# Optimization experiments

Measured on AMD Instinct MI355X. Metric: run time of the kernel, lower is better.

The kernel has to match this reference:

```python
import jax, jax.numpy as jnp
import numpy as np

B, C, H, W = 4, 512, 64, 64
KEY_DIM, VALUE_DIM = 512, 512


def setup_inputs() -> dict:
    key = jax.random.key(0)
    k1, k2, k3, k4 = jax.random.split(key, 4)
    s = 1.0 / np.sqrt(C).astype(np.float32)
    x = jax.random.normal(k1, (B, C, H, W), jnp.float32)
    # torch nn.Linear weights have shape (out_features, in_features)
    Wk = jax.random.normal(k2, (KEY_DIM, C), jnp.float32) * s
    Wq = jax.random.normal(k3, (KEY_DIM, C), jnp.float32) * s
    Wv = jax.random.normal(k4, (VALUE_DIM, C), jnp.float32) * s
    return {"x": x, "Wk": Wk, "Wq": Wq, "Wv": Wv}


def reference(x, Wk, Wq, Wv):
    b, c, h, w = x.shape
    kd = Wk.shape[0]
    n = h * w
    # (b,c,h,w) -> (b, n, c) tokens, matching transpose+flatten in the original
    xt = x.transpose(0, 2, 3, 1).reshape(b, n, c)
    q = xt @ Wq.T  # (b, n, kd)
    k = xt @ Wk.T  # (b, n, kd)
    v = xt @ Wv.T  # (b, n, vd)
    scaling = np.sqrt(float(kd)).astype(np.float32)
    scores = jax.nn.softmax(jnp.einsum('bnd,bmd->bnm', q, k) / scaling, axis=-1)
    # original: output[j] = sum_i values[i] * scores[j, i]  ==  scores @ V
    out = jnp.einsum('bnm,bmv->bnv', scores, v)  # (b, n, vd)
    # original scores_out: sum over dim=0 (query index) of the (n, n) score matrix
    scores_out = scores.sum(axis=1).reshape(b, 1, h, w)
    out = out.reshape(b, h, w, -1).transpose(0, 3, 1, 2)  # (b, vd, h, w)
    return out, scores_out
```

## Files before the change

### kernel.cpp

```cpp
#include <hip/hip_runtime.h>


typedef short bf16x8 __attribute__((ext_vector_type(8)));
typedef float f32x4 __attribute__((ext_vector_type(4)));

#define NTOK 4096
#define DDIM 512
#define NB   4

__device__ __forceinline__ unsigned short f32_bf16(float f) {
  union { float f; unsigned u; } v; v.f = f;
  unsigned r = v.u + 0x7FFFu + ((v.u >> 16) & 1u);
  return (unsigned short)(r >> 16);
}

__device__ __forceinline__ float bf16_f32(short s) {
  union { unsigned u; float f; } v;
  v.u = ((unsigned)(unsigned short)s) << 16;
  return v.f;
}

__global__ __launch_bounds__(256, 4) void qkv_proj(
    const float* __restrict__ x,
    const float* __restrict__ Wq,
    const float* __restrict__ Wk,
    const float* __restrict__ Wv,
    unsigned short* __restrict__ Qt,
    unsigned short* __restrict__ Kf,
    unsigned short* __restrict__ Vt)
{
  const int nt0 = blockIdx.x * 64;
  const int d0  = blockIdx.y * 64;
  const int b   = blockIdx.z;
  const int tid = threadIdx.x;
  const int wave = tid >> 6;
  const int lane = tid & 63;
  const int l15  = lane & 15;
  const int quad = lane >> 4;

  __shared__ __align__(16) unsigned short Xt[64 * 40];
  __shared__ __align__(16) unsigned short Wl[3][64 * 40];

  f32x4 aq[4], ak[4], av[4];
#pragma unroll
  for (int i = 0; i < 4; ++i) {
    aq[i] = (f32x4){0.f,0.f,0.f,0.f};
    ak[i] = (f32x4){0.f,0.f,0.f,0.f};
    av[i] = (f32x4){0.f,0.f,0.f,0.f};
  }

  const float* xb = x + (size_t)b * DDIM * NTOK + nt0;
  const int xn  = tid & 63;
  const int xc8 = tid >> 6;
  const int wc8 = tid & 3;
  const int wdd = tid >> 2;

  for (int cc = 0; cc < DDIM; cc += 32) {
    __syncthreads();
    {
      bf16x8 t;
#pragma unroll
      for (int j = 0; j < 8; ++j)
        t[j] = (short)f32_bf16(xb[(size_t)(cc + xc8 * 8 + j) * NTOK + xn]);
      *(bf16x8*)(&Xt[xn * 40 + xc8 * 8]) = t;
    }
    {
      const float* wsrc[3] = {Wq, Wk, Wv};
#pragma unroll
      for (int m = 0; m < 3; ++m) {
        const float* src = wsrc[m] + (size_t)(d0 + wdd) * DDIM + cc + wc8 * 8;
        bf16x8 t;
#pragma unroll
        for (int j = 0; j < 8; ++j) t[j] = (short)f32_bf16(src[j]);
        *(bf16x8*)(&Wl[m][wdd * 40 + wc8 * 8]) = t;
      }
    }
    __syncthreads();

    bf16x8 xa  = *(const bf16x8*)(&Xt[(wave * 16 + l15) * 40 + quad * 8]);
    bf16x8 wva = *(const bf16x8*)(&Wl[2][(wave * 16 + l15) * 40 + quad * 8]);
#pragma unroll
    for (int nt = 0; nt < 4; ++nt) {
      bf16x8 wqf = *(const bf16x8*)(&Wl[0][(nt * 16 + l15) * 40 + quad * 8]);
      bf16x8 wkf = *(const bf16x8*)(&Wl[1][(nt * 16 + l15) * 40 + quad * 8]);
      bf16x8 xbf = *(const bf16x8*)(&Xt[(nt * 16 + l15) * 40 + quad * 8]);
      aq[nt] = __builtin_amdgcn_mfma_f32_16x16x32_bf16(xa,  wqf, aq[nt], 0, 0, 0);
      ak[nt] = __builtin_amdgcn_mfma_f32_16x16x32_bf16(xa,  wkf, ak[nt], 0, 0, 0);
      av[nt] = __builtin_amdgcn_mfma_f32_16x16x32_bf16(wva, xbf, av[nt], 0, 0, 0);
    }
  }

#pragma unroll
  for (int nt = 0; nt < 4; ++nt) {
#pragma unroll
    for (int r = 0; r < 4; ++r) {
      const int tokq = nt0 + wave * 16 + quad * 4 + r;
      const int dq   = d0 + nt * 16 + l15;
      Qt[((size_t)b * NTOK + tokq) * DDIM + dq] = f32_bf16(aq[nt][r]);
      {
        const int kblk  = (nt0 >> 4) + wave;
        const int dc    = (d0 >> 5) + (nt >> 1);
        const int laneK = ((nt & 1) * 2 + (l15 >> 3)) * 16 + quad * 4 + r;
        Kf[((size_t)(b * 256 + kblk) * 16 + dc) * 512 + laneK * 8 + (l15 & 7)] =
            f32_bf16(ak[nt][r]);
      }
      const int dblk  = (d0 >> 4) + wave;
      const int ic    = (nt0 >> 5) + (nt >> 1);
      const int laneV = ((nt & 1) * 2 + (l15 >> 3)) * 16 + quad * 4 + r;
      Vt[(size_t)b * DDIM * NTOK +
         ((size_t)(dblk * 128 + ic) * 64 + laneV) * 8 + (l15 & 7)] =
          f32_bf16(av[nt][r]);
    }
  }
}

#define SCALE 0.044194173824159216f

__global__ __launch_bounds__(256, 2) void attn_lsum_p(
    const unsigned short* __restrict__ Qt,
    const unsigned short* __restrict__ Kf,
    unsigned short* __restrict__ Pt,
    float* __restrict__ lsum_g)
{
  const int qb = blockIdx.x;
  const int kp = blockIdx.y;
  const int b  = blockIdx.z;
  const int tid  = threadIdx.x;
  const int wave = tid >> 6;
  const int lane = tid & 63;
  const int l15  = lane & 15;
  const int quad = lane >> 4;
  const int q0   = qb * 128 + wave * 32;

  __shared__ __align__(16) unsigned short Klds[64 * 512];

  bf16x8 qf[2][16];
#pragma unroll
  for (int qt = 0; qt < 2; ++qt) {
    const unsigned short* qp =
        Qt + ((size_t)b * NTOK + q0 + qt * 16 + l15) * DDIM + quad * 8;
#pragma unroll
    for (int dc = 0; dc < 16; ++dc) qf[qt][dc] = *(const bf16x8*)(qp + dc * 32);
  }

  unsigned short* Pq = Pt + (size_t)b * NTOK * NTOK +
                       (size_t)(qb * 2 + (wave >> 1)) * 262144;
  const int ntb = (wave & 1) * 2;

  float ls[2][4] = {{0.f,0.f,0.f,0.f},{0.f,0.f,0.f,0.f}};

  for (int kc = 0; kc < 16; ++kc) {
    const int kblk0 = kp * 64 + kc * 4;
    __syncthreads();
    {
      const unsigned short* src = Kf + ((size_t)(b * 256 + kblk0) * 16) * 512;
#pragma unroll
      for (int it = 0; it < 16; ++it) {
        const int idx = (tid + it * 256) * 8;
        *(bf16x8*)(&Klds[idx]) = *(const bf16x8*)(src + idx);
      }
    }
    __syncthreads();

#pragma unroll
    for (int kt = 0; kt < 4; ++kt) {
      const int kabs = kblk0 + kt;
      f32x4 s0 = (f32x4){0.f,0.f,0.f,0.f};
      f32x4 s1 = (f32x4){0.f,0.f,0.f,0.f};
#pragma unroll
      for (int dc = 0; dc < 16; ++dc) {
        const bf16x8 kbf = *(const bf16x8*)(&Klds[(kt * 16 + dc) * 512 + lane * 8]);
        s0 = __builtin_amdgcn_mfma_f32_16x16x32_bf16(qf[0][dc], kbf, s0, 0, 0, 0);
        s1 = __builtin_amdgcn_mfma_f32_16x16x32_bf16(qf[1][dc], kbf, s1, 0, 0, 0);
      }
      const int ic    = kabs >> 1;
      const int lt_hi = ((kabs & 1) * 2 + (l15 >> 3)) * 16;
      const int jj    = l15 & 7;
#pragma unroll
      for (int r = 0; r < 4; ++r) {
        const float e0 = __expf(s0[r] * SCALE);
        const float e1 = __expf(s1[r] * SCALE);
        ls[0][r] += e0;
        ls[1][r] += e1;
        Pq[((size_t)(ic * 4 + ntb) * 64 + lt_hi + quad * 4 + r) * 8 + jj] =
            f32_bf16(e0);
        Pq[((size_t)(ic * 4 + ntb + 1) * 64 + lt_hi + quad * 4 + r) * 8 + jj] =
            f32_bf16(e1);
      }
    }
  }

#pragma unroll
  for (int qt = 0; qt < 2; ++qt)
#pragma unroll
    for (int r = 0; r < 4; ++r) {
      float v = ls[qt][r];
      v += __shfl_xor(v, 1);
      v += __shfl_xor(v, 2);
      v += __shfl_xor(v, 4);
      v += __shfl_xor(v, 8);
      if (l15 == 0)
        unsafeAtomicAdd(&lsum_g[(size_t)b * NTOK + q0 + qt * 16 + quad * 4 + r], v);
    }
}

__global__ __launch_bounds__(256, 2) void attn_pv(
    const unsigned short* __restrict__ Pt,
    const unsigned short* __restrict__ Vt,
    const float* __restrict__ lsum_g,
    float* __restrict__ out)
{
  const int q0b   = blockIdx.x;
  const int dpart = blockIdx.y;
  const int b     = blockIdx.z;
  const int tid  = threadIdx.x;
  const int wave = tid >> 6;
  const int lane = tid & 63;
  const int l15  = lane & 15;
  const int quad = lane >> 4;

  const int dblk0 = dpart * 16 + wave * 4;
  const unsigned short* Pq =
      Pt + (size_t)b * NTOK * NTOK + (size_t)q0b * 262144 + lane * 8;
  const unsigned short* Vb =
      Vt + (size_t)b * DDIM * NTOK + lane * 8;

  float rlv[4];
#pragma unroll
  for (int nt = 0; nt < 4; ++nt)
    rlv[nt] = 1.0f / lsum_g[(size_t)b * NTOK + q0b * 64 + nt * 16 + l15];

  f32x4 o[4][4];
#pragma unroll
  for (int i = 0; i < 4; ++i)
#pragma unroll
    for (int j = 0; j < 4; ++j) o[i][j] = (f32x4){0.f,0.f,0.f,0.f};

  bf16x8 pc[4], vc[4], pn[4], vn[4];
#pragma unroll
  for (int nt = 0; nt < 4; ++nt)
    pc[nt] = *(const bf16x8*)(Pq + (size_t)nt * 512);
#pragma unroll
  for (int mt = 0; mt < 4; ++mt)
    vc[mt] = *(const bf16x8*)(Vb + (size_t)(dblk0 + mt) * 65536);

#pragma unroll 2
  for (int ic = 0; ic < 127; ++ic) {
#pragma unroll
    for (int nt = 0; nt < 4; ++nt)
      pn[nt] = *(const bf16x8*)(Pq + (size_t)(ic + 1) * 2048 + (size_t)nt * 512);
#pragma unroll
    for (int mt = 0; mt < 4; ++mt)
      vn[mt] = *(const bf16x8*)(Vb + (size_t)(dblk0 + mt) * 65536 + (size_t)(ic + 1) * 512);
#pragma unroll
    for (int mt = 0; mt < 4; ++mt)
#pragma unroll
      for (int nt = 0; nt < 4; ++nt)
        o[mt][nt] = __builtin_amdgcn_mfma_f32_16x16x32_bf16(vc[mt], pc[nt], o[mt][nt], 0, 0, 0);
#pragma unroll
    for (int nt = 0; nt < 4; ++nt) pc[nt] = pn[nt];
#pragma unroll
    for (int mt = 0; mt < 4; ++mt) vc[mt] = vn[mt];
  }
#pragma unroll
  for (int mt = 0; mt < 4; ++mt)
#pragma unroll
    for (int nt = 0; nt < 4; ++nt)
      o[mt][nt] = __builtin_amdgcn_mfma_f32_16x16x32_bf16(vc[mt], pc[nt], o[mt][nt], 0, 0, 0);

  float* ob = out + ((size_t)b * DDIM + dpart * 256 + wave * 64) * NTOK + q0b * 64;
#pragma unroll
  for (int mt = 0; mt < 4; ++mt)
#pragma unroll
    for (int nt = 0; nt < 4; ++nt)
#pragma unroll
      for (int r = 0; r < 4; ++r)
        ob[(size_t)(mt * 16 + quad * 4 + r) * NTOK + nt * 16 + l15] =
            o[mt][nt][r] * rlv[nt];
}

__global__ __launch_bounds__(256, 4) void colsum_k(
    const unsigned short* __restrict__ Pt,
    const float* __restrict__ lsum_g,
    float* __restrict__ scores_out)
{
  const int ic = blockIdx.x;
  const int b  = blockIdx.y;
  const int tid = threadIdx.x;
  const int wave = tid >> 6;
  const int lane = tid & 63;
  const int l15  = lane & 15;
  const int quad = lane >> 4;

  __shared__ float red[4][32];

  const unsigned short* Pb = Pt + (size_t)b * NTOK * NTOK + (size_t)ic * 2048 + lane * 8;
  const float* lb = lsum_g + (size_t)b * NTOK;

  float acc[8];
#pragma unroll
  for (int j = 0; j < 8; ++j) acc[j] = 0.f;

  for (int q0b = wave; q0b < 64; q0b += 4) {
    const unsigned short* src = Pb + (size_t)q0b * 262144;
#pragma unroll
    for (int nt = 0; nt < 4; ++nt) {
      const bf16x8 p = *(const bf16x8*)(src + (size_t)nt * 512);
      const float rl = 1.0f / lb[q0b * 64 + nt * 16 + l15];
#pragma unroll
      for (int j = 0; j < 8; ++j) acc[j] = fmaf(bf16_f32(p[j]), rl, acc[j]);
    }
  }
#pragma unroll
  for (int j = 0; j < 8; ++j) {
    float v = acc[j];
    v += __shfl_xor(v, 1);
    v += __shfl_xor(v, 2);
    v += __shfl_xor(v, 4);
    v += __shfl_xor(v, 8);
    acc[j] = v;
  }
  if (l15 == 0) {
#pragma unroll
    for (int j = 0; j < 8; ++j) red[wave][quad * 8 + j] = acc[j];
  }
  __syncthreads();
  if (tid < 32)
    scores_out[(size_t)b * NTOK + ic * 32 + tid] =
        red[0][tid] + red[1][tid] + red[2][tid] + red[3][tid];
}

extern "C" void kernel_launch(void* const* d_in, const int* in_sizes, int n_in,
                              void* d_out, int out_size, void* d_ws, size_t ws_size,
                              hipStream_t stream) {
  const float* x  = (const float*)d_in[0];
  const float* Wk = (const float*)d_in[1];
  const float* Wq = (const float*)d_in[2];
  const float* Wv = (const float*)d_in[3];

  float* out = (float*)d_out;
  float* scores_out = out + (size_t)NB * DDIM * NTOK;

  const size_t mat_elems = (size_t)NB * NTOK * DDIM;
  unsigned short* Qt = (unsigned short*)d_ws;
  unsigned short* Kf = Qt + mat_elems;
  unsigned short* Vt = Kf + mat_elems;
  float* lbuf = (float*)(Vt + mat_elems);
  unsigned short* Pt = (unsigned short*)(lbuf + (size_t)NB * NTOK);

  hipMemsetAsync(lbuf, 0, (size_t)NB * NTOK * sizeof(float), stream);

  dim3 g1(NTOK / 64, DDIM / 64, NB);
  qkv_proj<<<g1, 256, 0, stream>>>(x, Wq, Wk, Wv, Qt, Kf, Vt);

  dim3 g2(NTOK / 128, 4, NB);
  attn_lsum_p<<<g2, 256, 0, stream>>>(Qt, Kf, Pt, lbuf);

  dim3 g3(NTOK / 64, 2, NB);
  attn_pv<<<g3, 256, 0, stream>>>(Pt, Vt, lbuf, out);

  dim3 g4(128, NB);
  colsum_k<<<g4, 256, 0, stream>>>(Pt, lbuf, scores_out);
}
```

Baseline: 358.6 us.

## Fuse column-sum into PV kernel and shrink per-wave output tile

Removes the separate colsum kernel by computing the softmax column sums inside attn_pv, with each P chunk summed by exactly one wave and accumulated via atomics into a zero-initialized scores buffer. The PV tile per wave is halved (2 d-blocks instead of 4), the grid doubles along the d dimension, and launch bounds allow higher occupancy, with explicit double-buffered loads. This saves one kernel launch and the dedicated pass over P for column sums. In exchange each P tile is now read by twice as many blocks, and atomics plus an extra memset are added.

```diff
diff --git a/kernel.cpp b/kernel.cpp
--- a/kernel.cpp
+++ b/kernel.cpp
@@ -204,11 +204,12 @@
     }
 }
 
-__global__ __launch_bounds__(256, 2) void attn_pv(
+__global__ __launch_bounds__(256, 4) void attn_pv(
     const unsigned short* __restrict__ Pt,
     const unsigned short* __restrict__ Vt,
     const float* __restrict__ lsum_g,
-    float* __restrict__ out)
+    float* __restrict__ out,
+    float* __restrict__ scores_out)
 {
   const int q0b   = blockIdx.x;
   const int dpart = blockIdx.y;
@@ -219,115 +220,96 @@
   const int l15  = lane & 15;
   const int quad = lane >> 4;
 
-  const int dblk0 = dpart * 16 + wave * 4;
+  const int dblk0 = dpart * 8 + wave * 2;
   const unsigned short* Pq =
       Pt + (size_t)b * NTOK * NTOK + (size_t)q0b * 262144 + lane * 8;
-  const unsigned short* Vb =
-      Vt + (size_t)b * DDIM * NTOK + lane * 8;
+  const unsigned short* Vp0 =
+      Vt + (size_t)b * DDIM * NTOK + (size_t)(dblk0 + 0) * 65536 + lane * 8;
+  const unsigned short* Vp1 =
+      Vt + (size_t)b * DDIM * NTOK + (size_t)(dblk0 + 1) * 65536 + lane * 8;
+  float* scb = scores_out + (size_t)b * NTOK;
 
   float rlv[4];
 #pragma unroll
   for (int nt = 0; nt < 4; ++nt)
     rlv[nt] = 1.0f / lsum_g[(size_t)b * NTOK + q0b * 64 + nt * 16 + l15];
 
-  f32x4 o[4][4];
-#pragma unroll
-  for (int i = 0; i < 4; ++i)
+  f32x4 o[2][4];
+#pragma unroll
+  for (int i = 0; i < 2; ++i)
 #pragma unroll
     for (int j = 0; j < 4; ++j) o[i][j] = (f32x4){0.f,0.f,0.f,0.f};
 
-  bf16x8 pc[4], vc[4], pn[4], vn[4];
-#pragma unroll
-  for (int nt = 0; nt < 4; ++nt)
-    pc[nt] = *(const bf16x8*)(Pq + (size_t)nt * 512);
-#pragma unroll
-  for (int mt = 0; mt < 4; ++mt)
-    vc[mt] = *(const bf16x8*)(Vb + (size_t)(dblk0 + mt) * 65536);
-
-#pragma unroll 2
-  for (int ic = 0; ic < 127; ++ic) {
-#pragma unroll
-    for (int nt = 0; nt < 4; ++nt)
-      pn[nt] = *(const bf16x8*)(Pq + (size_t)(ic + 1) * 2048 + (size_t)nt * 512);
-#pragma unroll
-    for (int mt = 0; mt < 4; ++mt)
-      vn[mt] = *(const bf16x8*)(Vb + (size_t)(dblk0 + mt) * 65536 + (size_t)(ic + 1) * 512);
-#pragma unroll
-    for (int mt = 0; mt < 4; ++mt)
-#pragma unroll
-      for (int nt = 0; nt < 4; ++nt)
-        o[mt][nt] = __builtin_amdgcn_mfma_f32_16x16x32_bf16(vc[mt], pc[nt], o[mt][nt], 0, 0, 0);
-#pragma unroll
-    for (int nt = 0; nt < 4; ++nt) pc[nt] = pn[nt];
-#pragma unroll
-    for (int mt = 0; mt < 4; ++mt) vc[mt] = vn[mt];
-  }
-#pragma unroll
-  for (int mt = 0; mt < 4; ++mt)
-#pragma unroll
-    for (int nt = 0; nt < 4; ++nt)
-      o[mt][nt] = __builtin_amdgcn_mfma_f32_16x16x32_bf16(vc[mt], pc[nt], o[mt][nt], 0, 0, 0);
-
-  float* ob = out + ((size_t)b * DDIM + dpart * 256 + wave * 64) * NTOK + q0b * 64;
-#pragma unroll
-  for (int mt = 0; mt < 4; ++mt)
+  bf16x8 pA[4], pB[4], vA[2], vB[2];
+
+#define LOADP(D_, IC_)                                                         \
+  do {                                                                         \
+    _Pragma("unroll") for (int nt = 0; nt < 4; ++nt)                           \
+      D_[nt] = *(const bf16x8*)(Pq + (size_t)(IC_)*2048 + nt * 512);           \
+  } while (0)
+
+#define LOADV(D_, IC_)                                                         \
+  do {                                                                         \
+    D_[0] = *(const bf16x8*)(Vp0 + (size_t)(IC_)*512);                         \
+    D_[1] = *(const bf16x8*)(Vp1 + (size_t)(IC_)*512);                         \
+  } while (0)
+
+#define PV_COMPUTE(P_, V_, IC_)                                                \
+  do {                                                                         \
+    _Pragma("unroll") for (int mt = 0; mt < 2; ++mt)                           \
+      _Pragma("unroll") for (int nt = 0; nt < 4; ++nt)                         \
+        o[mt][nt] = __builtin_amdgcn_mfma_f32_16x16x32_bf16(                   \
+            V_[mt], P_[nt], o[mt][nt], 0, 0, 0);                               \
+    if ((((IC_) >> 5) == dpart) && ((((IC_) >> 3) & 3) == wave)) {             \
+      float cj[8];                                                             \
+      _Pragma("unroll") for (int j = 0; j < 8; ++j) cj[j] = 0.f;               \
+      _Pragma("unroll") for (int nt = 0; nt < 4; ++nt)                         \
+        _Pragma("unroll") for (int j = 0; j < 8; ++j)                          \
+          cj[j] = fmaf(bf16_f32(P_[nt][j]), rlv[nt], cj[j]);                   \
+      _Pragma("unroll") for (int j = 0; j < 8; ++j) {                          \
+        float v_ = cj[j];                                                      \
+        v_ += __shfl_xor(v_, 1);                                               \
+        v_ += __shfl_xor(v_, 2);                                               \
+        v_ += __shfl_xor(v_, 4);                                               \
+        v_ += __shfl_xor(v_, 8);                                               \
+        cj[j] = v_;                                                            \
+      }                                                                        \
+      if (l15 == 0) {                                                          \
+        _Pragma("unroll") for (int j = 0; j < 8; ++j)                          \
+          unsafeAtomicAdd(&scb[(IC_)*32 + quad * 8 + j], cj[j]);               \
+      }                                                                        \
+    }                                                                          \
+  } while (0)
+
+  LOADP(pA, 0); LOADV(vA, 0);
+  LOADP(pB, 1); LOADV(vB, 1);
+
+  for (int ic = 0; ic < 124; ic += 2) {
+    PV_COMPUTE(pA, vA, ic);
+    LOADP(pA, ic + 2); LOADV(vA, ic + 2);
+    PV_COMPUTE(pB, vB, ic + 1);
+    LOADP(pB, ic + 3); LOADV(vB, ic + 3);
+  }
+  PV_COMPUTE(pA, vA, 124);
+  LOADP(pA, 126); LOADV(vA, 126);
+  PV_COMPUTE(pB, vB, 125);
+  LOADP(pB, 127); LOADV(vB, 127);
+  PV_COMPUTE(pA, vA, 126);
+  PV_COMPUTE(pB, vB, 127);
+
+#undef LOADP
+#undef LOADV
+#undef PV_COMPUTE
+
+  float* ob = out + ((size_t)b * DDIM + dpart * 128 + wave * 32) * NTOK + q0b * 64;
+#pragma unroll
+  for (int mt = 0; mt < 2; ++mt)
 #pragma unroll
     for (int nt = 0; nt < 4; ++nt)
 #pragma unroll
       for (int r = 0; r < 4; ++r)
         ob[(size_t)(mt * 16 + quad * 4 + r) * NTOK + nt * 16 + l15] =
             o[mt][nt][r] * rlv[nt];
-}
-
-__global__ __launch_bounds__(256, 4) void colsum_k(
-    const unsigned short* __restrict__ Pt,
-    const float* __restrict__ lsum_g,
-    float* __restrict__ scores_out)
-{
-  const int ic = blockIdx.x;
-  const int b  = blockIdx.y;
-  const int tid = threadIdx.x;
-  const int wave = tid >> 6;
-  const int lane = tid & 63;
-  const int l15  = lane & 15;
-  const int quad = lane >> 4;
-
-  __shared__ float red[4][32];
-
-  const unsigned short* Pb = Pt + (size_t)b * NTOK * NTOK + (size_t)ic * 2048 + lane * 8;
-  const float* lb = lsum_g + (size_t)b * NTOK;
-
-  float acc[8];
-#pragma unroll
-  for (int j = 0; j < 8; ++j) acc[j] = 0.f;
-
-  for (int q0b = wave; q0b < 64; q0b += 4) {
-    const unsigned short* src = Pb + (size_t)q0b * 262144;
-#pragma unroll
-    for (int nt = 0; nt < 4; ++nt) {
-      const bf16x8 p = *(const bf16x8*)(src + (size_t)nt * 512);
-      const float rl = 1.0f / lb[q0b * 64 + nt * 16 + l15];
-#pragma unroll
-      for (int j = 0; j < 8; ++j) acc[j] = fmaf(bf16_f32(p[j]), rl, acc[j]);
-    }
-  }
-#pragma unroll
-  for (int j = 0; j < 8; ++j) {
-    float v = acc[j];
-    v += __shfl_xor(v, 1);
-    v += __shfl_xor(v, 2);
-    v += __shfl_xor(v, 4);
-    v += __shfl_xor(v, 8);
-    acc[j] = v;
-  }
-  if (l15 == 0) {
-#pragma unroll
-    for (int j = 0; j < 8; ++j) red[wave][quad * 8 + j] = acc[j];
-  }
-  __syncthreads();
-  if (tid < 32)
-    scores_out[(size_t)b * NTOK + ic * 32 + tid] =
-        red[0][tid] + red[1][tid] + red[2][tid] + red[3][tid];
 }
 
 extern "C" void kernel_launch(void* const* d_in, const int* in_sizes, int n_in,
@@ -349,6 +331,7 @@
   unsigned short* Pt = (unsigned short*)(lbuf + (size_t)NB * NTOK);
 
   hipMemsetAsync(lbuf, 0, (size_t)NB * NTOK * sizeof(float), stream);
+  hipMemsetAsync(scores_out, 0, (size_t)NB * NTOK * sizeof(float), stream);
 
   dim3 g1(NTOK / 64, DDIM / 64, NB);
   qkv_proj<<<g1, 256, 0, stream>>>(x, Wq, Wk, Wv, Qt, Kf, Vt);
@@ -356,9 +339,6 @@
   dim3 g2(NTOK / 128, 4, NB);
   attn_lsum_p<<<g2, 256, 0, stream>>>(Qt, Kf, Pt, lbuf);
 
-  dim3 g3(NTOK / 64, 2, NB);
-  attn_pv<<<g3, 256, 0, stream>>>(Pt, Vt, lbuf, out);
-
-  dim3 g4(128, NB);
-  colsum_k<<<g4, 256, 0, stream>>>(Pt, lbuf, scores_out);
-}
+  dim3 g3(NTOK / 64, 4, NB);
+  attn_pv<<<g3, 256, 0, stream>>>(Pt, Vt, lbuf, out, scores_out);
+}
```

Result: slower. 404.8 us (+12.9%).

## Double-buffer K and P tiles in LDS via async global_load_lds

Applied to the files above, without the earlier changes.

The QK^T kernel now stages K chunks into a double-buffered LDS array with direct global-to-LDS loads, so the next chunk is prefetched while MFMAs run on the current one. This replaces two barriers per chunk with one. The PV kernel stops loading P straight into registers from global memory and instead stages P tiles through double-buffered LDS with async loads. V fragments are kept in two rotating register sets. This adds 64KB of LDS per block in the PV kernel, which may lower occupancy.

```diff
diff --git a/kernel.cpp b/kernel.cpp
--- a/kernel.cpp
+++ b/kernel.cpp
@@ -18,6 +18,13 @@
   union { unsigned u; float f; } v;
   v.u = ((unsigned)(unsigned short)s) << 16;
   return v.f;
+}
+
+__device__ __forceinline__ void gload_lds16(const unsigned short* g,
+                                            unsigned short* l) {
+  __builtin_amdgcn_global_load_lds(
+      (__attribute__((address_space(1))) void*)(g),
+      (__attribute__((address_space(3))) void*)(l), 16, 0, 0);
 }
 
 __global__ __launch_bounds__(256, 4) void qkv_proj(
@@ -132,7 +139,7 @@
   const int quad = lane >> 4;
   const int q0   = qb * 128 + wave * 32;
 
-  __shared__ __align__(16) unsigned short Klds[64 * 512];
+  __shared__ __align__(16) unsigned short Klds[2][16384];
 
   bf16x8 qf[2][16];
 #pragma unroll
@@ -149,27 +156,33 @@
 
   float ls[2][4] = {{0.f,0.f,0.f,0.f},{0.f,0.f,0.f,0.f}};
 
-  for (int kc = 0; kc < 16; ++kc) {
-    const int kblk0 = kp * 64 + kc * 4;
-    __syncthreads();
-    {
-      const unsigned short* src = Kf + ((size_t)(b * 256 + kblk0) * 16) * 512;
-#pragma unroll
-      for (int it = 0; it < 16; ++it) {
-        const int idx = (tid + it * 256) * 8;
-        *(bf16x8*)(&Klds[idx]) = *(const bf16x8*)(src + idx);
-      }
-    }
-    __syncthreads();
-
-#pragma unroll
-    for (int kt = 0; kt < 4; ++kt) {
-      const int kabs = kblk0 + kt;
+  const unsigned short* Ksrc0 = Kf + ((size_t)(b * 256 + kp * 64) * 16) * 512;
+
+#define KSTAGE(KC_, B_)                                                        \
+  do {                                                                         \
+    const unsigned short* ks_ = Ksrc0 + (size_t)(KC_)*16384;                   \
+    _Pragma("unroll") for (int c_ = 0; c_ < 8; ++c_) {                         \
+      const int ch_ = c_ * 4 + wave;                                           \
+      gload_lds16(ks_ + ch_ * 512 + lane * 8, &Klds[B_][ch_ * 512]);           \
+    }                                                                          \
+  } while (0)
+
+  KSTAGE(0, 0);
+  __syncthreads();
+
+  for (int kc2 = 0; kc2 < 32; ++kc2) {
+    const int cb = kc2 & 1;
+    if (kc2 < 31) KSTAGE(kc2 + 1, cb ^ 1);
+
+#pragma unroll
+    for (int kt = 0; kt < 2; ++kt) {
+      const int kabs = kp * 64 + kc2 * 2 + kt;
       f32x4 s0 = (f32x4){0.f,0.f,0.f,0.f};
       f32x4 s1 = (f32x4){0.f,0.f,0.f,0.f};
 #pragma unroll
       for (int dc = 0; dc < 16; ++dc) {
-        const bf16x8 kbf = *(const bf16x8*)(&Klds[(kt * 16 + dc) * 512 + lane * 8]);
+        const bf16x8 kbf =
+            *(const bf16x8*)(&Klds[cb][(kt * 16 + dc) * 512 + lane * 8]);
         s0 = __builtin_amdgcn_mfma_f32_16x16x32_bf16(qf[0][dc], kbf, s0, 0, 0, 0);
         s1 = __builtin_amdgcn_mfma_f32_16x16x32_bf16(qf[1][dc], kbf, s1, 0, 0, 0);
       }
@@ -188,7 +201,9 @@
             f32_bf16(e1);
       }
     }
-  }
+    __syncthreads();
+  }
+#undef KSTAGE
 
 #pragma unroll
   for (int qt = 0; qt < 2; ++qt)
@@ -221,10 +236,12 @@
 
   const int dblk0 = dpart * 16 + wave * 4;
   const unsigned short* Pq =
-      Pt + (size_t)b * NTOK * NTOK + (size_t)q0b * 262144 + lane * 8;
+      Pt + (size_t)b * NTOK * NTOK + (size_t)q0b * 262144;
   const unsigned short* Vb =
       Vt + (size_t)b * DDIM * NTOK + lane * 8;
 
+  __shared__ __align__(16) unsigned short Plds[2][16384];
+
   float rlv[4];
 #pragma unroll
   for (int nt = 0; nt < 4; ++nt)
@@ -236,37 +253,61 @@
 #pragma unroll
     for (int j = 0; j < 4; ++j) o[i][j] = (f32x4){0.f,0.f,0.f,0.f};
 
-  bf16x8 pc[4], vc[4], pn[4], vn[4];
-#pragma unroll
-  for (int nt = 0; nt < 4; ++nt)
-    pc[nt] = *(const bf16x8*)(Pq + (size_t)nt * 512);
-#pragma unroll
-  for (int mt = 0; mt < 4; ++mt)
-    vc[mt] = *(const bf16x8*)(Vb + (size_t)(dblk0 + mt) * 65536);
-
-#pragma unroll 2
-  for (int ic = 0; ic < 127; ++ic) {
-#pragma unroll
-    for (int nt = 0; nt < 4; ++nt)
-      pn[nt] = *(const bf16x8*)(Pq + (size_t)(ic + 1) * 2048 + (size_t)nt * 512);
-#pragma unroll
-    for (int mt = 0; mt < 4; ++mt)
-      vn[mt] = *(const bf16x8*)(Vb + (size_t)(dblk0 + mt) * 65536 + (size_t)(ic + 1) * 512);
-#pragma unroll
-    for (int mt = 0; mt < 4; ++mt)
+  bf16x8 vA[4], vB[4];
+
+#define LOADVN(D_, IC_)                                                        \
+  do {                                                                         \
+    _Pragma("unroll") for (int mt = 0; mt < 4; ++mt)                           \
+      D_[mt] = *(const bf16x8*)(Vb + (size_t)(dblk0 + mt) * 65536 +            \
+                                (size_t)(IC_)*512);                            \
+  } while (0)
+
+#define PSTAGE(S_, B_)                                                         \
+  do {                                                                         \
+    const unsigned short* ps_ = Pq + (size_t)(S_)*16384;                       \
+    _Pragma("unroll") for (int c_ = 0; c_ < 8; ++c_) {                         \
+      const int ch_ = c_ * 4 + wave;                                           \
+      gload_lds16(ps_ + ch_ * 512 + lane * 8, &Plds[B_][ch_ * 512]);           \
+    }                                                                          \
+  } while (0)
+
+  LOADVN(vA, 0);
+  LOADVN(vB, 1);
+  PSTAGE(0, 0);
+  __syncthreads();
+
+  for (int s = 0; s < 16; ++s) {
+    const int cb = s & 1;
+    if (s < 15) PSTAGE(s + 1, cb ^ 1);
+#pragma unroll
+    for (int i = 0; i < 8; ++i) {
+      const int ic = s * 8 + i;
+      bf16x8 pb[4];
 #pragma unroll
       for (int nt = 0; nt < 4; ++nt)
-        o[mt][nt] = __builtin_amdgcn_mfma_f32_16x16x32_bf16(vc[mt], pc[nt], o[mt][nt], 0, 0, 0);
-#pragma unroll
-    for (int nt = 0; nt < 4; ++nt) pc[nt] = pn[nt];
-#pragma unroll
-    for (int mt = 0; mt < 4; ++mt) vc[mt] = vn[mt];
-  }
-#pragma unroll
-  for (int mt = 0; mt < 4; ++mt)
-#pragma unroll
-    for (int nt = 0; nt < 4; ++nt)
-      o[mt][nt] = __builtin_amdgcn_mfma_f32_16x16x32_bf16(vc[mt], pc[nt], o[mt][nt], 0, 0, 0);
+        pb[nt] = *(const bf16x8*)(&Plds[cb][i * 2048 + nt * 512 + lane * 8]);
+      if ((i & 1) == 0) {
+#pragma unroll
+        for (int mt = 0; mt < 4; ++mt)
+#pragma unroll
+          for (int nt = 0; nt < 4; ++nt)
+            o[mt][nt] = __builtin_amdgcn_mfma_f32_16x16x32_bf16(
+                vA[mt], pb[nt], o[mt][nt], 0, 0, 0);
+        if (ic + 2 < 128) LOADVN(vA, ic + 2);
+      } else {
+#pragma unroll
+        for (int mt = 0; mt < 4; ++mt)
+#pragma unroll
+          for (int nt = 0; nt < 4; ++nt)
+            o[mt][nt] = __builtin_amdgcn_mfma_f32_16x16x32_bf16(
+                vB[mt], pb[nt], o[mt][nt], 0, 0, 0);
+        if (ic + 2 < 128) LOADVN(vB, ic + 2);
+      }
+    }
+    __syncthreads();
+  }
+#undef LOADVN
+#undef PSTAGE
 
   float* ob = out + ((size_t)b * DDIM + dpart * 256 + wave * 64) * NTOK + q0b * 64;
 #pragma unroll
```

After: 354.1 us. About the same (-1.2%).
